# Performance work log

Measured on AMD Instinct MI355X. Metric: run time of the kernel, lower is better.

## Reference

```python
import jax, jax.numpy as jnp
import numpy as np

B, K, H, W = 16, 32, 28, 28   # batch, set size, image h, image w
HID, OUT = 64, 64             # hid_dim, out_dim
NOPS = 8                      # permutation-equivariant 3->3 pool/broadcast basis ops


def setup_inputs() -> dict:
    key = jax.random.key(0)
    ks = jax.random.split(key, 8)
    def p(k, shape, fan_in):
        return jax.random.normal(k, shape, jnp.float32) / np.float32(np.sqrt(fan_in))
    return dict(
        x=jax.random.normal(ks[0], (B, K, H, W), jnp.float32),
        conv1_w=p(ks[1], (32, 1, 3, 3), 9),
        conv1_b=jnp.zeros((32,), jnp.float32),
        conv2_w=p(ks[2], (64, 32, 3, 3), 32 * 9),
        conv2_b=jnp.zeros((64,), jnp.float32),
        fc_w=p(ks[3], (HID, 64 * 7 * 7), 64 * 7 * 7),
        fc_b=jnp.zeros((HID,), jnp.float32),
        eq_w=p(ks[4], (HID, OUT, NOPS), HID * NOPS),
        eq_b=jnp.zeros((OUT,), jnp.float32),
        out_w=p(ks[5], (1, OUT), OUT),
        out_b=jnp.zeros((1,), jnp.float32),
    )


def _conv2d(x, w, b):
    y = jax.lax.conv_general_dilated(x, w, (1, 1), 'SAME',
                                     dimension_numbers=('NCHW', 'OIHW', 'NCHW'))
    return y + b[None, :, None, None]


def _maxpool2(x):
    return jax.lax.reduce_window(x, -jnp.inf, jax.lax.max,
                                 (1, 1, 2, 2), (1, 1, 2, 2), 'VALID')


def _forward(x, conv1_w, conv1_b, conv2_w, conv2_b, fc_w, fc_b, eq_w, eq_b, out_w, out_b):
    # --- BasicConvNet embed: (B*K, 1, H, W) -> (B*K, HID) ---
    x1 = x.reshape(B * K, 1, H, W)
    h1 = _maxpool2(jax.nn.relu(_conv2d(x1, conv1_w, conv1_b)))   # (B*K, 32, 14, 14)
    h2 = _maxpool2(jax.nn.relu(_conv2d(h1, conv2_w, conv2_b)))   # (B*K, 64, 7, 7)
    feat = jax.nn.relu(h2.reshape(B * K, -1) @ fc_w.T + fc_b)    # (B*K, HID)
    x4 = feat.reshape(B, K, HID)

    # --- triple outer product: (B, HID, K, K, K), no contracted index ---
    x5 = jnp.einsum('bid,bjd,bkd->bdijk', x4, x4, x4)

    # --- SetEq3to3: 8 equivariant pool/broadcast basis ops, contracted with eq_w[d,e,o].
    # Contract each pooled tensor with its slice of eq_w BEFORE broadcasting (same math,
    # avoids materializing 8 full (B,d,K,K,K) op tensors). ---
    m_i  = x5.mean(2)           # (B, d, j, k)
    m_j  = x5.mean(3)           # (B, d, i, k)
    m_k  = x5.mean(4)           # (B, d, i, j)
    m_ij = m_i.mean(2)          # (B, d, k)
    m_ik = m_i.mean(3)          # (B, d, j)
    m_jk = m_j.mean(3)          # (B, d, i)
    m_all = m_ij.mean(2)        # (B, d)

    x6 = (jnp.einsum('bdijk,de->beijk', x5, eq_w[:, :, 0])
          + jnp.einsum('bdjk,de->bejk', m_i, eq_w[:, :, 1])[:, :, None, :, :]
          + jnp.einsum('bdik,de->beik', m_j, eq_w[:, :, 2])[:, :, :, None, :]
          + jnp.einsum('bdij,de->beij', m_k, eq_w[:, :, 3])[:, :, :, :, None]
          + jnp.einsum('bdk,de->bek', m_ij, eq_w[:, :, 4])[:, :, None, None, :]
          + jnp.einsum('bdj,de->bej', m_ik, eq_w[:, :, 5])[:, :, None, :, None]
          + jnp.einsum('bdi,de->bei', m_jk, eq_w[:, :, 6])[:, :, :, None, None]
          + jnp.einsum('bd,de->be', m_all, eq_w[:, :, 7])[:, :, None, None, None]
          + eq_b[None, :, None, None, None])          # (B, OUT, K, K, K)

    # permute to channels-last, relu, pool over (i,j,k), relu, final linear
    x7 = jax.nn.relu(x6.transpose(0, 2, 3, 4, 1))     # (B, K, K, K, OUT)
    x8 = x7.mean(axis=(1, 2, 3))                      # (B, OUT)
    x9 = jax.nn.relu(x8)
    # dropout_prob = 0 -> identity
    return x9 @ out_w.T + out_b                       # (B, 1)


def reference(x, conv1_w, conv1_b, conv2_w, conv2_b, fc_w, fc_b, eq_w, eq_b, out_w, out_b):
    return _forward(x, conv1_w, conv1_b, conv2_w, conv2_b, fc_w, fc_b,
                    eq_w, eq_b, out_w, out_b)
```

## Files before the change

### kernel.cpp

```cpp
#include <hip/hip_runtime.h>
#include <hip/hip_bf16.h>


typedef __attribute__((ext_vector_type(8))) short short8;
typedef __attribute__((ext_vector_type(4))) float f32x4;

__device__ __forceinline__ f32x4 mfma_bf16(short8 a, short8 b, f32x4 c) {
  return __builtin_amdgcn_mfma_f32_16x16x32_bf16(a, b, c, 0, 0, 0);
}

__device__ __forceinline__ unsigned short f2bs(float f) {
  unsigned int u = __float_as_uint(f);
  unsigned int r = u + 0x7fffu + ((u >> 16) & 1u);
  return (unsigned short)(r >> 16);
}
__device__ __forceinline__ unsigned int pk2(float x, float y) {
  union { __hip_bfloat162 h; unsigned int u; } cv;
  cv.h = __float22bfloat162_rn(make_float2(x, y));
  return cv.u;
}
__device__ __forceinline__ void stb4(short* p, float4 v) {
  *(unsigned int*)(p)     = pk2(v.x, v.y);
  *(unsigned int*)(p + 2) = pk2(v.z, v.w);
}

__global__ __launch_bounds__(256, 2) void k12_conv(const float* __restrict__ x,
    const float* __restrict__ w1, const float* __restrict__ b1,
    const float* __restrict__ w2, const float* __restrict__ b2,
    short* __restrict__ h2b,
    const float* __restrict__ eqw, float* __restrict__ Wt,
    const float* __restrict__ fcw, short* __restrict__ fcwb) {
  const int n = blockIdx.x, t = threadIdx.x;
  if (n >= 512) {
    if (n < 520) {
      const int m = n - 512;
      for (int idx = t; idx < 4096; idx += 256) {
        int e = idx >> 6, d = idx & 63;
        Wt[m*4096 + idx] = eqw[d*512 + e*8 + m];
      }
    } else {
      int base = (n - 520)*12544 + t;
      for (int q = 0; q < 49; ++q) {
        int idx = base + q*256;
        fcwb[idx] = (short)f2bs(fcw[idx]);
      }
    }
    return;
  }
  __shared__ float si[30*30];
  __shared__ float sw[32*9];
  __shared__ float sb[32];
  __shared__ __align__(16) short inT[16*18*40];
  const int wv = t >> 6, l = t & 63, quad = l >> 4, col = l & 15;

  const int c_out = wv*16 + col;
  float w72[72];
  {
    const float4* src = (const float4*)(w2 + c_out*288 + quad*72);
#pragma unroll
    for (int q = 0; q < 18; ++q) {
      float4 v = src[q];
      w72[q*4+0] = v.x; w72[q*4+1] = v.y; w72[q*4+2] = v.z; w72[q*4+3] = v.w;
    }
  }
  union SU { short8 v; unsigned int u[4]; };
  short8 Bq[9];
#pragma unroll
  for (int dd = 0; dd < 9; ++dd) {
    SU b;
#pragma unroll
    for (int q = 0; q < 4; ++q)
      b.u[q] = pk2(w72[(2*q)*9 + dd], w72[(2*q+1)*9 + dd]);
    Bq[dd] = b.v;
  }
  const float bb2 = b2[c_out];

  for (int idx = t; idx < 900; idx += 256) si[idx] = 0.f;
  {
    unsigned int* zp = (unsigned int*)inT;
    for (int idx = t; idx < 5760; idx += 256) zp[idx] = 0u;
  }
  for (int idx = t; idx < 288; idx += 256) sw[idx] = w1[idx];
  if (t < 32) sb[t] = b1[t];
  __syncthreads();
  for (int idx = t; idx < 784; idx += 256) {
    int y = idx / 28, xx = idx - y*28;
    si[(y+1)*30 + xx + 1] = x[n*784 + idx];
  }
  __syncthreads();

  {
    const int cg = t & 7;
    float wreg[4][9], breg[4];
#pragma unroll
    for (int cc = 0; cc < 4; ++cc) {
      breg[cc] = sb[cg*4 + cc];
#pragma unroll
      for (int q = 0; q < 9; ++q) wreg[cc][q] = sw[(cg*4 + cc)*9 + q];
    }
    for (int idx = t; idx < 1568; idx += 256) {
      int pos = idx >> 3;
      int py = pos / 14, px = pos - py*14;
      float pt[4][4];
#pragma unroll
      for (int r = 0; r < 4; ++r)
#pragma unroll
        for (int q = 0; q < 4; ++q)
          pt[r][q] = si[(2*py + r)*30 + 2*px + q];
      float res[4];
#pragma unroll
      for (int cc = 0; cc < 4; ++cc) {
        float best = 0.f;
#pragma unroll
        for (int a = 0; a < 2; ++a)
#pragma unroll
          for (int b3 = 0; b3 < 2; ++b3) {
            float v = breg[cc]
              + wreg[cc][0]*pt[a+0][b3+0] + wreg[cc][1]*pt[a+0][b3+1] + wreg[cc][2]*pt[a+0][b3+2]
              + wreg[cc][3]*pt[a+1][b3+0] + wreg[cc][4]*pt[a+1][b3+1] + wreg[cc][5]*pt[a+1][b3+2]
              + wreg[cc][6]*pt[a+2][b3+0] + wreg[cc][7]*pt[a+2][b3+1] + wreg[cc][8]*pt[a+2][b3+2];
            best = fmaxf(best, v);
          }
        res[cc] = best;
      }
      uint2 pkd;
      pkd.x = pk2(res[0], res[1]);
      pkd.y = pk2(res[2], res[3]);
      *(uint2*)&inT[(py+1)*720 + (px+1)*40 + cg*4] = pkd;
    }
  }
  __syncthreads();

  for (int p = 0; p < 7; ++p) {
    short8 Ar[4][3];
#pragma unroll
    for (int rr = 0; rr < 4; ++rr)
#pragma unroll
      for (int dx = 0; dx < 3; ++dx)
        Ar[rr][dx] = *(const short8*)&inT[(2*p + rr)*720 + (col + dx)*40 + quad*8];
    f32x4 a0 = {0.f,0.f,0.f,0.f}, a1 = {0.f,0.f,0.f,0.f};
#pragma unroll
    for (int dy = 0; dy < 3; ++dy)
#pragma unroll
      for (int dx = 0; dx < 3; ++dx) {
        a0 = mfma_bf16(Ar[dy][dx],     Bq[dy*3 + dx], a0);
        a1 = mfma_bf16(Ar[dy + 1][dx], Bq[dy*3 + dx], a1);
      }
#pragma unroll
    for (int a = 0; a < 2; ++a) {
      int px = quad*2 + a;
      if (px < 7) {
        float m0 = fmaxf(fmaxf(a0[2*a], a0[2*a + 1]), fmaxf(a1[2*a], a1[2*a + 1]));
        h2b[n*3136 + c_out*49 + p*7 + px] = (short)f2bs(fmaxf(m0 + bb2, 0.f));
      }
    }
  }
}

__global__ __launch_bounds__(256) void k3_mfma(const short* __restrict__ h2b,
    const short* __restrict__ fcwb, float* __restrict__ part) {
  const int blk = blockIdx.x, kp = blockIdx.y, t = threadIdx.x;
  const int w = t >> 6, l = t & 63, quad = l >> 4, col = l & 15;
  const int mt = w & 1, nh = w >> 1;
  const int img = blk*32 + mt*16 + col;
  const short* Ap = h2b + img*3136 + kp*224 + quad*8;
  const short* B0 = fcwb + (nh*32 + col)*3136 + kp*224 + quad*8;
  const short* B1 = fcwb + (nh*32 + 16 + col)*3136 + kp*224 + quad*8;
  f32x4 acc0 = {0.f,0.f,0.f,0.f}, acc1 = {0.f,0.f,0.f,0.f};
#pragma unroll
  for (int q = 0; q < 7; ++q) {
    short8 A  = *(const short8*)(Ap + q*32);
    short8 b0 = *(const short8*)(B0 + q*32);
    short8 b1 = *(const short8*)(B1 + q*32);
    acc0 = mfma_bf16(A, b0, acc0);
    acc1 = mfma_bf16(A, b1, acc1);
  }
  const int e0 = nh*32 + col, e1 = e0 + 16;
  const int base = blk*32 + mt*16 + quad*4;
  float* dst = part + kp*32768;
#pragma unroll
  for (int r = 0; r < 4; ++r) {
    dst[(base + r)*64 + e0] = acc0[r];
    dst[(base + r)*64 + e1] = acc1[r];
  }
}

__global__ __launch_bounds__(256) void k4_prep(const float* __restrict__ part,
    const float* __restrict__ fb, const float* __restrict__ Wt,
    const float* __restrict__ eqb, float* __restrict__ feat,
    float* __restrict__ s, float* __restrict__ t7c, float* __restrict__ x8,
    int* __restrict__ cnt) {
  __shared__ __align__(16) float sf[2048];
  __shared__ float ss[64];
  const int b = blockIdx.x, t = threadIdx.x;
  for (int v4 = t; v4 < 512; v4 += 256) {
    float4 a = {0.f, 0.f, 0.f, 0.f};
#pragma unroll
    for (int kp = 0; kp < 14; ++kp) {
      float4 p = *(const float4*)&part[kp*32768 + b*2048 + v4*4];
      a.x += p.x; a.y += p.y; a.z += p.z; a.w += p.w;
    }
    float4 fbv = *(const float4*)&fb[(v4*4) & 63];
    float4 r;
    r.x = fmaxf(a.x + fbv.x, 0.f);
    r.y = fmaxf(a.y + fbv.y, 0.f);
    r.z = fmaxf(a.z + fbv.z, 0.f);
    r.w = fmaxf(a.w + fbv.w, 0.f);
    *(float4*)&sf[v4*4] = r;
    *(float4*)&feat[b*2048 + v4*4] = r;
  }
  __syncthreads();
  if (t < 64) {
    float a = 0.f;
    for (int i = 0; i < 32; ++i) a += sf[i*64 + t];
    a *= (1.f/32.f);
    s[b*64 + t] = a;
    ss[t] = a;
  }
  __syncthreads();
  if (t < 64) {
    const float* W7 = Wt + 7*4096 + t*64;
    float t7 = 0.f;
    for (int d = 0; d < 64; ++d) {
      float sv = ss[d];
      t7 += sv*sv*sv * W7[d];
    }
    t7c[b*64 + t] = t7 + eqb[t];
    x8[b*64 + t] = 0.f;
  }
  if (t == 0) cnt[b] = 0;
}

__global__ __launch_bounds__(256, 2) void k5_mfma(const float* __restrict__ feat,
    const float* __restrict__ s_, const float* __restrict__ Wt,
    const float* __restrict__ t7c, float* __restrict__ x8, int* __restrict__ cnt,
    const float* __restrict__ ow, const float* __restrict__ ob,
    float* __restrict__ out) {
  __shared__ __align__(16) float Fm[32*68];
  __shared__ __align__(16) float FI[64];
  __shared__ __align__(16) float SV[64];
  __shared__ __align__(16) float C0[64];
  __shared__ float C0P[128];
  __shared__ float KCf[32*68];
  __shared__ float JCf[32*68];
  __shared__ float RED[256];
  __shared__ int isLast;
  __shared__ __align__(16) short Fb[32*72];
  __shared__ __align__(16) short QPb[64*72];
  __shared__ __align__(16) short G2b[64*72];
  __shared__ __align__(16) short G3b[64*72];

  const int i = blockIdx.x, b = blockIdx.y, t = threadIdx.x;
  const int w = t >> 6, l = t & 63, quad = l >> 4, col = l & 15;

  for (int idx = t; idx < 2048; idx += 256) {
    int r = idx >> 6, d = idx & 63;
    float v = feat[b*2048 + idx];
    Fm[r*68 + d] = v;
    Fb[r*72 + d] = (short)f2bs(v);
  }
  if (t < 64) { FI[t] = feat[b*2048 + i*64 + t]; SV[t] = s_[b*64 + t]; }
  __syncthreads();

  {
    const int e = t >> 2, dbase = (t & 3) * 16;
    const float* W0 = Wt + 0*4096 + e*64;
    const float* W1 = Wt + 1*4096 + e*64;
    const float* W2 = Wt + 2*4096 + e*64;
    const float* W3 = Wt + 3*4096 + e*64;
    const float* W4 = Wt + 4*4096 + e*64;
    const float* W5 = Wt + 5*4096 + e*64;
#pragma unroll
    for (int q = 0; q < 4; ++q) {
      int off = dbase + q*4;
      float4 fi4 = *(const float4*)&FI[off];
      float4 sv4 = *(const float4*)&SV[off];
      float4 w0 = *(const float4*)&W0[off];
      float4 w1 = *(const float4*)&W1[off];
      float4 w2 = *(const float4*)&W2[off];
      float4 w3 = *(const float4*)&W3[off];
      float4 w4 = *(const float4*)&W4[off];
      float4 w5 = *(const float4*)&W5[off];
      float4 qp = fi4*w0 + sv4*w1;
      float4 g2 = sv4*(fi4*w2 + sv4*w4);
      float4 g3 = sv4*(fi4*w3 + sv4*w5);
      stb4(&QPb[e*72 + off], qp);
      stb4(&G2b[e*72 + off], g2);
      stb4(&G3b[e*72 + off], g3);
    }
  }
  if (t < 128) {
    int e = t & 63, dh = t >> 6;
    const float* W6 = Wt + 6*4096 + e*64 + dh*32;
    const float* fip = FI + dh*32;
    const float* svp = SV + dh*32;
    float a = 0.f;
#pragma unroll
    for (int dd = 0; dd < 32; ++dd) {
      float sd = svp[dd];
      a += sd*sd*fip[dd]*W6[dd];
    }
    C0P[dh*64 + e] = a;
  }
  __syncthreads();

  if (w < 2) {
    const short* G = w ? G3b : G2b;
    float* DST = w ? JCf : KCf;
    short8 Bf[4][2];
#pragma unroll
    for (int n = 0; n < 4; ++n)
#pragma unroll
      for (int s2 = 0; s2 < 2; ++s2)
        Bf[n][s2] = *(const short8*)&G[(n*16 + col)*72 + s2*32 + quad*8];
#pragma unroll
    for (int m = 0; m < 2; ++m) {
      short8 A0 = *(const short8*)&Fb[(m*16 + col)*72 + quad*8];
      short8 A1 = *(const short8*)&Fb[(m*16 + col)*72 + 32 + quad*8];
#pragma unroll
      for (int n = 0; n < 4; ++n) {
        f32x4 z = {0.f, 0.f, 0.f, 0.f};
        f32x4 ac = mfma_bf16(A1, Bf[n][1], mfma_bf16(A0, Bf[n][0], z));
#pragma unroll
        for (int r = 0; r < 4; ++r)
          DST[(m*16 + quad*4 + r)*68 + n*16 + col] = ac[r];
      }
    }
  } else if (w == 2) {
    C0[l] = C0P[l] + C0P[64 + l] + t7c[b*64 + l];
  }
  __syncthreads();

  float c0v[4];
#pragma unroll
  for (int n = 0; n < 4; ++n) c0v[n] = C0[n*16 + col];
  float jcq[8][4];
#pragma unroll
  for (int jj = 0; jj < 8; ++jj)
#pragma unroll
    for (int n = 0; n < 4; ++n)
      jcq[jj][n] = JCf[(w*8 + jj)*68 + n*16 + col] + c0v[n];
  float kcv[2][4][4];
#pragma unroll
  for (int kb2 = 0; kb2 < 2; ++kb2)
#pragma unroll
    for (int r = 0; r < 4; ++r)
#pragma unroll
      for (int n = 0; n < 4; ++n)
        kcv[kb2][r][n] = KCf[(kb2*16 + quad*4 + r)*68 + n*16 + col];
  short8 Bq[4][2];
#pragma unroll
  for (int n = 0; n < 4; ++n)
#pragma unroll
    for (int s2 = 0; s2 < 2; ++s2)
      Bq[n][s2] = *(const short8*)&QPb[(n*16 + col)*72 + s2*32 + quad*8];

  float4 fkv[2][4];
#pragma unroll
  for (int kb2 = 0; kb2 < 2; ++kb2) {
    const float* fk = &Fm[(kb2*16 + col)*68 + quad*8];
    fkv[kb2][0] = *(const float4*)(fk);
    fkv[kb2][1] = *(const float4*)(fk + 4);
    fkv[kb2][2] = *(const float4*)(fk + 32);
    fkv[kb2][3] = *(const float4*)(fk + 36);
  }

  float sum[4] = {0.f, 0.f, 0.f, 0.f};
  union SU { short8 v; unsigned int u[4]; };

#pragma unroll
  for (int jj = 0; jj < 8; ++jj) {
    const float* fj = &Fm[(w*8 + jj)*68 + quad*8];
    float4 j0 = *(const float4*)(fj);
    float4 j1 = *(const float4*)(fj + 4);
    float4 j2 = *(const float4*)(fj + 32);
    float4 j3 = *(const float4*)(fj + 36);
#pragma unroll
    for (int kb2 = 0; kb2 < 2; ++kb2) {
      float4 k0 = fkv[kb2][0], k1 = fkv[kb2][1];
      float4 k2v = fkv[kb2][2], k3v = fkv[kb2][3];
      SU A0, A1;
      A0.u[0] = pk2(j0.x*k0.x, j0.y*k0.y);
      A0.u[1] = pk2(j0.z*k0.z, j0.w*k0.w);
      A0.u[2] = pk2(j1.x*k1.x, j1.y*k1.y);
      A0.u[3] = pk2(j1.z*k1.z, j1.w*k1.w);
      A1.u[0] = pk2(j2.x*k2v.x, j2.y*k2v.y);
      A1.u[1] = pk2(j2.z*k2v.z, j2.w*k2v.w);
      A1.u[2] = pk2(j3.x*k3v.x, j3.y*k3v.y);
      A1.u[3] = pk2(j3.z*k3v.z, j3.w*k3v.w);
      f32x4 ac[4];
#pragma unroll
      for (int n = 0; n < 4; ++n) {
        f32x4 z = {0.f, 0.f, 0.f, 0.f};
        ac[n] = mfma_bf16(A1.v, Bq[n][1], mfma_bf16(A0.v, Bq[n][0], z));
      }
#pragma unroll
      for (int n = 0; n < 4; ++n)
#pragma unroll
        for (int r = 0; r < 4; ++r) {
          float v = ac[n][r] + kcv[kb2][r][n] + jcq[jj][n];
          sum[n] += fmaxf(v, 0.f);
        }
    }
  }

#pragma unroll
  for (int n = 0; n < 4; ++n) {
    float v = sum[n];
    v += __shfl_xor(v, 16, 64);
    v += __shfl_xor(v, 32, 64);
    if (l < 16) RED[w*64 + n*16 + l] = v;
  }
  __syncthreads();
  if (t < 64) {
    float tot = RED[t] + RED[64 + t] + RED[128 + t] + RED[192 + t];
    atomicAdd(&x8[b*64 + t], tot);
  }
  __syncthreads();
  if (t == 0) {
    __threadfence();
    int old = atomicAdd(&cnt[b], 1);
    isLast = (old == 31);
  }
  __syncthreads();
  if (isLast) {
    __threadfence();
    if (t < 64) {
      float xv = atomicAdd(&x8[b*64 + t], 0.0f);
      float v = fmaxf(xv * (1.f/32768.f), 0.f) * ow[t];
#pragma unroll
      for (int off = 32; off > 0; off >>= 1) v += __shfl_down(v, off, 64);
      if (t == 0) out[b] = v + ob[0];
    }
  }
}

extern "C" void kernel_launch(void* const* d_in, const int* in_sizes, int n_in,
                              void* d_out, int out_size, void* d_ws, size_t ws_size,
                              hipStream_t stream) {
  const float* x   = (const float*)d_in[0];
  const float* c1w = (const float*)d_in[1];
  const float* c1b = (const float*)d_in[2];
  const float* c2w = (const float*)d_in[3];
  const float* c2b = (const float*)d_in[4];
  const float* fcw = (const float*)d_in[5];
  const float* fcb = (const float*)d_in[6];
  const float* eqw = (const float*)d_in[7];
  const float* eqb = (const float*)d_in[8];
  const float* ow  = (const float*)d_in[9];
  const float* ob  = (const float*)d_in[10];
  float* out = (float*)d_out;

  short* h2b  = (short*)d_ws;
  float* feat = (float*)(h2b + 512*3136);
  float* s    = feat + 512*64;
  float* t7c  = s + 1024;
  float* x8   = t7c + 1024;
  int*   cnt  = (int*)(x8 + 1024);
  float* Wt   = (float*)(cnt + 16);
  short* fcwb = (short*)(Wt + 32768);
  float* part = (float*)(fcwb + 200704);

  hipLaunchKernelGGL(k12_conv, dim3(536), dim3(256), 0, stream,
                     x, c1w, c1b, c2w, c2b, h2b, eqw, Wt, fcw, fcwb);
  hipLaunchKernelGGL(k3_mfma,  dim3(16, 14), dim3(256), 0, stream, h2b, fcwb, part);
  hipLaunchKernelGGL(k4_prep,  dim3(16),  dim3(256), 0, stream,
                     part, fcb, Wt, eqb, feat, s, t7c, x8, cnt);
  hipLaunchKernelGGL(k5_mfma,  dim3(32, 16), dim3(256), 0, stream,
                     feat, s, Wt, t7c, x8, cnt, ow, ob, out);
}
```

Measured before the change: 141.6 us.

## Store eq weights as bf16 and replace atomic finalize with separate reduction kernel

Stores the equivariant weight slices 0-6 as bf16 during the prep kernel, which halves the weight bytes k5 loads per block, and unpacks them with shifts. Slice 7 stays fp32. The atomicAdd, counter and last-block finalize logic in k5 is replaced by per-block partial writes plus a small k6_out kernel that reduces the 32 partials per batch. This removes the atomics, the thread fences and the extra syncs, but adds one more kernel launch and rounds the weights to bf16 for precision.

```diff
diff --git a/kernel.cpp b/kernel.cpp
--- a/kernel.cpp
+++ b/kernel.cpp
@@ -19,16 +19,19 @@
   cv.h = __float22bfloat162_rn(make_float2(x, y));
   return cv.u;
 }
-__device__ __forceinline__ void stb4(short* p, float4 v) {
-  *(unsigned int*)(p)     = pk2(v.x, v.y);
-  *(unsigned int*)(p + 2) = pk2(v.z, v.w);
+__device__ __forceinline__ void ub8(const short* p, float* f) {
+  uint4 u = *(const uint4*)p;
+  f[0] = __uint_as_float(u.x << 16); f[1] = __uint_as_float(u.x & 0xffff0000u);
+  f[2] = __uint_as_float(u.y << 16); f[3] = __uint_as_float(u.y & 0xffff0000u);
+  f[4] = __uint_as_float(u.z << 16); f[5] = __uint_as_float(u.z & 0xffff0000u);
+  f[6] = __uint_as_float(u.w << 16); f[7] = __uint_as_float(u.w & 0xffff0000u);
 }
 
 __global__ __launch_bounds__(256, 2) void k12_conv(const float* __restrict__ x,
     const float* __restrict__ w1, const float* __restrict__ b1,
     const float* __restrict__ w2, const float* __restrict__ b2,
     short* __restrict__ h2b,
-    const float* __restrict__ eqw, float* __restrict__ Wt,
+    const float* __restrict__ eqw, float* __restrict__ W7t, short* __restrict__ Wtb,
     const float* __restrict__ fcw, short* __restrict__ fcwb) {
   const int n = blockIdx.x, t = threadIdx.x;
   if (n >= 512) {
@@ -36,7 +39,9 @@
       const int m = n - 512;
       for (int idx = t; idx < 4096; idx += 256) {
         int e = idx >> 6, d = idx & 63;
-        Wt[m*4096 + idx] = eqw[d*512 + e*8 + m];
+        float v = eqw[d*512 + e*8 + m];
+        if (m == 7) W7t[idx] = v;
+        else        Wtb[m*4096 + idx] = (short)f2bs(v);
       }
     } else {
       int base = (n - 520)*12544 + t;
@@ -186,10 +191,9 @@
 }
 
 __global__ __launch_bounds__(256) void k4_prep(const float* __restrict__ part,
-    const float* __restrict__ fb, const float* __restrict__ Wt,
+    const float* __restrict__ fb, const float* __restrict__ W7t,
     const float* __restrict__ eqb, float* __restrict__ feat,
-    float* __restrict__ s, float* __restrict__ t7c, float* __restrict__ x8,
-    int* __restrict__ cnt) {
+    float* __restrict__ s, float* __restrict__ t7c) {
   __shared__ __align__(16) float sf[2048];
   __shared__ float ss[64];
   const int b = blockIdx.x, t = threadIdx.x;
@@ -219,23 +223,19 @@
   }
   __syncthreads();
   if (t < 64) {
-    const float* W7 = Wt + 7*4096 + t*64;
+    const float* W7 = W7t + t*64;
     float t7 = 0.f;
     for (int d = 0; d < 64; ++d) {
       float sv = ss[d];
       t7 += sv*sv*sv * W7[d];
     }
     t7c[b*64 + t] = t7 + eqb[t];
-    x8[b*64 + t] = 0.f;
-  }
-  if (t == 0) cnt[b] = 0;
+  }
 }
 
 __global__ __launch_bounds__(256, 2) void k5_mfma(const float* __restrict__ feat,
-    const float* __restrict__ s_, const float* __restrict__ Wt,
-    const float* __restrict__ t7c, float* __restrict__ x8, int* __restrict__ cnt,
-    const float* __restrict__ ow, const float* __restrict__ ob,
-    float* __restrict__ out) {
+    const float* __restrict__ s_, const short* __restrict__ Wtb,
+    const float* __restrict__ t7c, float* __restrict__ x8p) {
   __shared__ __align__(16) float Fm[32*68];
   __shared__ __align__(16) float FI[64];
   __shared__ __align__(16) float SV[64];
@@ -244,7 +244,6 @@
   __shared__ float KCf[32*68];
   __shared__ float JCf[32*68];
   __shared__ float RED[256];
-  __shared__ int isLast;
   __shared__ __align__(16) short Fb[32*72];
   __shared__ __align__(16) short QPb[64*72];
   __shared__ __align__(16) short G2b[64*72];
@@ -264,41 +263,53 @@
 
   {
     const int e = t >> 2, dbase = (t & 3) * 16;
-    const float* W0 = Wt + 0*4096 + e*64;
-    const float* W1 = Wt + 1*4096 + e*64;
-    const float* W2 = Wt + 2*4096 + e*64;
-    const float* W3 = Wt + 3*4096 + e*64;
-    const float* W4 = Wt + 4*4096 + e*64;
-    const float* W5 = Wt + 5*4096 + e*64;
-#pragma unroll
-    for (int q = 0; q < 4; ++q) {
-      int off = dbase + q*4;
-      float4 fi4 = *(const float4*)&FI[off];
-      float4 sv4 = *(const float4*)&SV[off];
-      float4 w0 = *(const float4*)&W0[off];
-      float4 w1 = *(const float4*)&W1[off];
-      float4 w2 = *(const float4*)&W2[off];
-      float4 w3 = *(const float4*)&W3[off];
-      float4 w4 = *(const float4*)&W4[off];
-      float4 w5 = *(const float4*)&W5[off];
-      float4 qp = fi4*w0 + sv4*w1;
-      float4 g2 = sv4*(fi4*w2 + sv4*w4);
-      float4 g3 = sv4*(fi4*w3 + sv4*w5);
-      stb4(&QPb[e*72 + off], qp);
-      stb4(&G2b[e*72 + off], g2);
-      stb4(&G3b[e*72 + off], g3);
+#pragma unroll
+    for (int h = 0; h < 2; ++h) {
+      int off = dbase + h*8;
+      float w0[8], w1[8], w2[8], w3[8], w4[8], w5[8];
+      ub8(&Wtb[0*4096 + e*64 + off], w0);
+      ub8(&Wtb[1*4096 + e*64 + off], w1);
+      ub8(&Wtb[2*4096 + e*64 + off], w2);
+      ub8(&Wtb[3*4096 + e*64 + off], w3);
+      ub8(&Wtb[4*4096 + e*64 + off], w4);
+      ub8(&Wtb[5*4096 + e*64 + off], w5);
+      uint4 qv, g2v, g3v;
+      unsigned int* qp = &qv.x;
+      unsigned int* g2p = &g2v.x;
+      unsigned int* g3p = &g3v.x;
+#pragma unroll
+      for (int j = 0; j < 4; ++j) {
+        float fi0 = FI[off + 2*j],     fi1 = FI[off + 2*j + 1];
+        float s0  = SV[off + 2*j],     s1  = SV[off + 2*j + 1];
+        float q0 = fi0*w0[2*j]   + s0*w1[2*j];
+        float q1 = fi1*w0[2*j+1] + s1*w1[2*j+1];
+        float a0 = s0*(fi0*w2[2*j]   + s0*w4[2*j]);
+        float a1 = s1*(fi1*w2[2*j+1] + s1*w4[2*j+1]);
+        float c0 = s0*(fi0*w3[2*j]   + s0*w5[2*j]);
+        float c1 = s1*(fi1*w3[2*j+1] + s1*w5[2*j+1]);
+        qp[j]  = pk2(q0, q1);
+        g2p[j] = pk2(a0, a1);
+        g3p[j] = pk2(c0, c1);
+      }
+      *(uint4*)&QPb[e*72 + off] = qv;
+      *(uint4*)&G2b[e*72 + off] = g2v;
+      *(uint4*)&G3b[e*72 + off] = g3v;
     }
   }
   if (t < 128) {
     int e = t & 63, dh = t >> 6;
-    const float* W6 = Wt + 6*4096 + e*64 + dh*32;
-    const float* fip = FI + dh*32;
-    const float* svp = SV + dh*32;
+    const short* W6 = Wtb + 6*4096 + e*64 + dh*32;
     float a = 0.f;
 #pragma unroll
-    for (int dd = 0; dd < 32; ++dd) {
-      float sd = svp[dd];
-      a += sd*sd*fip[dd]*W6[dd];
+    for (int g = 0; g < 4; ++g) {
+      float wf[8];
+      ub8(&W6[g*8], wf);
+#pragma unroll
+      for (int dd = 0; dd < 8; ++dd) {
+        int d = dh*32 + g*8 + dd;
+        float sd = SV[d];
+        a += sd*sd*FI[d]*wf[dd];
+      }
     }
     C0P[dh*64 + e] = a;
   }
@@ -414,25 +425,21 @@
   __syncthreads();
   if (t < 64) {
     float tot = RED[t] + RED[64 + t] + RED[128 + t] + RED[192 + t];
-    atomicAdd(&x8[b*64 + t], tot);
-  }
-  __syncthreads();
-  if (t == 0) {
-    __threadfence();
-    int old = atomicAdd(&cnt[b], 1);
-    isLast = (old == 31);
-  }
-  __syncthreads();
-  if (isLast) {
-    __threadfence();
-    if (t < 64) {
-      float xv = atomicAdd(&x8[b*64 + t], 0.0f);
-      float v = fmaxf(xv * (1.f/32768.f), 0.f) * ow[t];
-#pragma unroll
-      for (int off = 32; off > 0; off >>= 1) v += __shfl_down(v, off, 64);
-      if (t == 0) out[b] = v + ob[0];
-    }
-  }
+    x8p[(b*32 + i)*64 + t] = tot;
+  }
+}
+
+__global__ __launch_bounds__(64) void k6_out(const float* __restrict__ x8p,
+    const float* __restrict__ ow, const float* __restrict__ ob,
+    float* __restrict__ out) {
+  const int bb = blockIdx.x, t = threadIdx.x;
+  float a = 0.f;
+#pragma unroll
+  for (int i = 0; i < 32; ++i) a += x8p[(bb*32 + i)*64 + t];
+  float v = fmaxf(a * (1.f/32768.f), 0.f) * ow[t];
+#pragma unroll
+  for (int off = 32; off > 0; off >>= 1) v += __shfl_down(v, off, 64);
+  if (t == 0) out[bb] = v + ob[0];
 }
 
 extern "C" void kernel_launch(void* const* d_in, const int* in_sizes, int n_in,
@@ -453,19 +460,19 @@
 
   short* h2b  = (short*)d_ws;
   float* feat = (float*)(h2b + 512*3136);
-  float* s    = feat + 512*64;
+  float* s    = feat + 32768;
   float* t7c  = s + 1024;
-  float* x8   = t7c + 1024;
-  int*   cnt  = (int*)(x8 + 1024);
-  float* Wt   = (float*)(cnt + 16);
-  short* fcwb = (short*)(Wt + 32768);
+  float* x8p  = t7c + 1024;
+  float* W7t  = x8p + 32768;
+  short* Wtb  = (short*)(W7t + 4096);
+  short* fcwb = Wtb + 7*4096;
   float* part = (float*)(fcwb + 200704);
 
   hipLaunchKernelGGL(k12_conv, dim3(536), dim3(256), 0, stream,
-                     x, c1w, c1b, c2w, c2b, h2b, eqw, Wt, fcw, fcwb);
+                     x, c1w, c1b, c2w, c2b, h2b, eqw, W7t, Wtb, fcw, fcwb);
   hipLaunchKernelGGL(k3_mfma,  dim3(16, 14), dim3(256), 0, stream, h2b, fcwb, part);
   hipLaunchKernelGGL(k4_prep,  dim3(16),  dim3(256), 0, stream,
-                     part, fcb, Wt, eqb, feat, s, t7c, x8, cnt);
-  hipLaunchKernelGGL(k5_mfma,  dim3(32, 16), dim3(256), 0, stream,
-                     feat, s, Wt, t7c, x8, cnt, ow, ob, out);
-}
+                     part, fcb, W7t, eqb, feat, s, t7c);
+  hipLaunchKernelGGL(k5_mfma,  dim3(32, 16), dim3(256), 0, stream, feat, s, Wtb, t7c, x8p);
+  hipLaunchKernelGGL(k6_out,   dim3(16),  dim3(64),  0, stream, x8p, ow, ob, out);
+}
```

Measured after the change: 122.3 us. -13.6%, faster.
